# Kernel tuning notes

Hardware: AMD Instinct MI355X
Metric: run time of the kernel (lower is better)

The kernel has to match this reference:

```python
import jax, jax.numpy as jnp
import numpy as np

B, T, F, H, K = 512, 128, 256, 512, 3

def setup_inputs() -> dict:
    key = jax.random.key(0)
    ks = jax.random.split(key, 8)
    x = jax.random.normal(ks[0], (B, T, F), dtype=jnp.float32)
    theta = jnp.ones((F,), dtype=jnp.float32)                 # selector logits
    Wx = jax.random.normal(ks[1], (F, H), dtype=jnp.float32) * 0.1
    Wh = jax.random.normal(ks[2], (H, H), dtype=jnp.float32) * 0.1
    b = jnp.zeros((H,), dtype=jnp.float32)
    c = jax.random.normal(ks[3], (H, K), dtype=jnp.float32)   # fuzzy centers
    sigma = jnp.ones((H, K), dtype=jnp.float32)               # fuzzy widths
    q = jax.random.normal(ks[4], (H, K), dtype=jnp.float32)   # rule consequents
    Wc = jax.random.normal(ks[5], (H, 1), dtype=jnp.float32) * 0.05  # classifier
    bc = jnp.zeros((1,), dtype=jnp.float32)
    return dict(x=x, theta=theta, Wx=Wx, Wh=Wh, b=b, c=c, sigma=sigma, q=q, Wc=Wc, bc=bc)


def reference(x, theta, Wx, Wh, b, c, sigma, q, Wc, bc):
    weights = jax.nn.sigmoid(theta)                 # [F]
    xf = x * weights                                # [B,T,F]
    # x_t @ Wx is used twice per step (for z_t and new_info); precompute once for all t.
    xw = jnp.einsum('btf,fh->bth', xf, Wx)          # [B,T,H]
    new_info = jnp.tanh(xw)                         # [B,T,H]
    inv_den = 1.0 / (2.0 * sigma ** 2 + 1e-8)       # [H,K]

    def step(h, inp):
        xw_t, new_t = inp                           # [B,H], [B,H]
        z = xw_t + h @ Wh + b                       # [B,H]
        mu = jnp.exp(-(z[..., None] - c) ** 2 * inv_den)   # [B,H,K]
        g = jax.nn.sigmoid(jnp.sum(mu * q, axis=-1) / (jnp.sum(mu, axis=-1) + 1e-8))
        h = (1.0 - g) * h + g * new_t
        return h, None

    h0 = jnp.zeros((x.shape[0], Wh.shape[0]), dtype=x.dtype)
    h, _ = jax.lax.scan(step, h0, (jnp.swapaxes(xw, 0, 1), jnp.swapaxes(new_info, 0, 1)))
    logits = h @ Wc + bc                            # [B,1]
    return logits, weights
```

## Files before the change

kernel.cpp:

```cpp
#include <hip/hip_runtime.h>
#include <hip/hip_bf16.h>


#define B_  512
#define T_  128
#define F_  256
#define H_  512
#define LOG2E 1.4426950408889634f

#define XW_T_STRIDE 262144

typedef __attribute__((ext_vector_type(8))) short short8;
typedef __attribute__((ext_vector_type(4))) float float4v;
typedef __attribute__((ext_vector_type(4))) int int4i;

__device__ inline ushort f2bf(float f) {
  __hip_bfloat16 h = __float2bfloat16(f);
  return *reinterpret_cast<ushort*>(&h);
}
__device__ inline float bf2f(unsigned u) { return __uint_as_float(u << 16); }
__device__ inline float fexp2(float x) { return __builtin_amdgcn_exp2f(x); }
__device__ inline float frcp(float x) { return __builtin_amdgcn_rcpf(x); }

#define WS_W2I8 67108864
#define WS_WXF  67371008
#define WS_GP8  67633152
#define WS_BVEC 67649536
#define WS_WCV  67651584
#define WS_SCOL 67653632
#define WS_WTS  67657728

__global__ __launch_bounds__(256) void prep_weights(
    const float* __restrict__ Wh, const float* __restrict__ Wx,
    const float* __restrict__ theta, const float* __restrict__ b,
    const float* __restrict__ c, const float* __restrict__ sigma,
    const float* __restrict__ q, const float* __restrict__ Wc,
    int* __restrict__ W2, ushort* __restrict__ WxF,
    float* __restrict__ scol, float* __restrict__ out_w,
    float* __restrict__ gp8, float* __restrict__ bvec,
    float* __restrict__ wcv, float* __restrict__ wts) {
  __shared__ float lds[16544];
  const int t = threadIdx.x;

  if (blockIdx.x < 32) {
    const int nb = blockIdx.x;
    const int cc = t & 15, rg = t >> 4;
    float m = 0.f;
#pragma unroll
    for (int s = 0; s < 32; ++s)
      m = fmaxf(m, fabsf(Wh[(rg + s * 16) * H_ + nb * 16 + cc]));
    lds[rg * 16 + cc] = m;
    __syncthreads();
    if (t < 16) {
      float mm = lds[t];
#pragma unroll
      for (int s = 1; s < 16; ++s) mm = fmaxf(mm, lds[s * 16 + t]);
      mm = fmaxf(mm, 1e-20f);
      scol[nb * 16 + t] = mm / (127.f * 127.f);
      lds[256 + t] = 127.f / mm;
    }
    __syncthreads();
    const int lane = t & 63, dw = t >> 6;
    const int n = nb * 16 + (lane & 15);
    const float iv = lds[256 + (lane & 15)];
#pragma unroll
    for (int kt = 0; kt < 8; ++kt) {
      int pk = 0;
#pragma unroll
      for (int jj = 0; jj < 4; ++jj) {
        const int k = kt * 64 + ((lane >> 4) << 4) + dw * 4 + jj;
        int qv = (int)rintf(Wh[k * H_ + n] * iv);
        qv = min(127, max(-127, qv));
        pk |= (qv & 255) << (8 * jj);
      }
      W2[((kt * 32 + nb) * 64 + lane) * 4 + dw] = pk;
    }
  } else if (blockIdx.x < 40) {
    const int kt = blockIdx.x - 32;
#pragma unroll
    for (int it = 0; it < 16; ++it) {
      const int lin = (it * 256 + t) * 4;
      const float4 v = *(const float4*)(Wx + kt * 32 * H_ + lin);
      const int f = lin >> 9, n0 = lin & 511;
      lds[f * 517 + n0 + 0] = v.x;
      lds[f * 517 + n0 + 1] = v.y;
      lds[f * 517 + n0 + 2] = v.z;
      lds[f * 517 + n0 + 3] = v.w;
    }
    __syncthreads();
#pragma unroll
    for (int it = 0; it < 8; ++it) {
      const int o = (it * 256 + t) * 8;
      const int lane = (o >> 3) & 63, nb = o >> 9;
      const int n = nb * 16 + (lane & 15), fb = (lane >> 4) << 3;
      ushort v[8];
#pragma unroll
      for (int j = 0; j < 8; ++j) v[j] = f2bf(lds[(fb + j) * 517 + n]);
      *(short8*)(WxF + kt * 16384 + o) = *(short8*)v;
    }
  } else {
#pragma unroll
    for (int r = 0; r < 2; ++r) {
      const int i = t + r * 256;
      if (i < F_) {
        float w = 1.f / (1.f + __expf(-theta[i]));
        out_w[i] = w;
        wts[i] = w;
      }
      float a[3], cc[3], qq[3];
#pragma unroll
      for (int k = 0; k < 3; ++k) {
        float s = sigma[i * 3 + k];
        cc[k] = c[i * 3 + k];
        a[k] = -LOG2E / (2.f * s * s + 1e-8f);
        qq[k] = q[i * 3 + k];
      }
      gp8[i * 8 + 0] = cc[0];
      gp8[i * 8 + 1] = cc[1];
      gp8[i * 8 + 2] = cc[2];
      gp8[i * 8 + 3] = a[0];
      gp8[i * 8 + 4] = a[1];
      gp8[i * 8 + 5] = a[2];
      gp8[i * 8 + 6] = __uint_as_float((unsigned)f2bf(qq[0]) |
                                       ((unsigned)f2bf(qq[1]) << 16));
      gp8[i * 8 + 7] = __uint_as_float((unsigned)f2bf(qq[2]));
      bvec[i] = b[i];
      wcv[i] = Wc[i];
    }
  }
}

__global__ __launch_bounds__(256, 1) void gemm1_kernel(
    const float* __restrict__ x, const float* __restrict__ wts,
    const ushort* __restrict__ WxF, ushort* __restrict__ xw2) {
  __shared__ ushort A[64 * 264];
  const int tid = threadIdx.x;
  const int lane = tid & 63, wg = tid >> 6;
  const int col16 = lane & 15, quad = lane >> 4;
  const int tt = blockIdx.x, bb = blockIdx.y;

  {
    const float4 wv = *(const float4*)(wts + lane * 4);
#pragma unroll
    for (int it = 0; it < 16; ++it) {
      const int row = it * 4 + wg;
      float4 xv = *(const float4*)(x + ((size_t)(bb * 64 + row) * T_ + tt) * F_ + lane * 4);
      ushort4 o;
      o.x = f2bf(xv.x * wv.x);
      o.y = f2bf(xv.y * wv.y);
      o.z = f2bf(xv.z * wv.z);
      o.w = f2bf(xv.w * wv.w);
      *(ushort4*)&A[row * 264 + lane * 4] = o;
    }
  }
  __syncthreads();

  const float4v zero = {0.f, 0.f, 0.f, 0.f};
#pragma unroll
  for (int nn = 0; nn < 2; ++nn) {
    float4v acc[16];
#pragma unroll
    for (int i = 0; i < 16; ++i) acc[i] = zero;
#pragma unroll
    for (int kt = 0; kt < 8; ++kt) {
      short8 af = *(const short8*)&A[(wg * 16 + col16) * 264 + kt * 32 + quad * 8];
      short8 bfv[16];
#pragma unroll
      for (int nt = 0; nt < 16; ++nt)
        bfv[nt] = *(const short8*)(WxF + ((kt * 32 + nn * 16 + nt) * 64 + lane) * 8);
#pragma unroll
      for (int nt = 0; nt < 16; ++nt)
        acc[nt] = __builtin_amdgcn_mfma_f32_16x16x32_bf16(af, bfv[nt], acc[nt], 0, 0, 0);
    }
#pragma unroll
    for (int nt = 0; nt < 16; ++nt) {
      ushort2 lo, hi;
      lo.x = f2bf(acc[nt][0]);
      lo.y = f2bf(acc[nt][1]);
      hi.x = f2bf(acc[nt][2]);
      hi.y = f2bf(acc[nt][3]);
      const int bg0 = bb * 32 + wg * 8 + quad * 2;
      const size_t off0 =
          (((size_t)tt * 256 + bg0) * 8 + nn * 4 + (nt >> 2)) * 128 +
          ((nt & 3) * 16 + col16) * 2;
      *(ushort2*)(xw2 + off0) = lo;
      *(ushort2*)(xw2 + off0 + 1024) = hi;
    }
  }
}

__global__ __launch_bounds__(512, 2) void scan4_kernel(
    const ushort* __restrict__ xw2, const int4i* __restrict__ W2,
    const float* __restrict__ gp8, const float* __restrict__ bvec,
    const float* __restrict__ wcv, const float* __restrict__ scol,
    const float* __restrict__ bc, float* __restrict__ out) {
  __shared__ __align__(16) char hb[2][1152];
  __shared__ float red[8][2];
  const int tid = threadIdx.x;
  const int lane = tid & 63, w = tid >> 6;
  const int col16 = lane & 15, quad = lane >> 4;
  const int bg = blockIdx.x;

  for (int i = tid; i < 576; i += 512) ((int*)hb)[i] = 0;

  int4i bfr[8][4];
#pragma unroll
  for (int kt = 0; kt < 8; ++kt)
#pragma unroll
    for (int nt = 0; nt < 4; ++nt)
      bfr[kt][nt] = W2[(kt * 32 + w * 4 + nt) * 64 + lane];

  const int col = w * 64 + lane;
  const float bcol = bvec[col], scl = scol[col], wcl = wcv[col];
  float4v g0 = *(const float4v*)(gp8 + col * 8);
  float4v g1 = *(const float4v*)(gp8 + col * 8 + 4);
  const float c0v = g0[0], c1v = g0[1], c2v = g0[2];
  const float a0v = g0[3], a1v = g1[0], a2v = g1[1];
  unsigned p01 = __float_as_uint(g1[2]);
  const float q0v = bf2f(p01 & 0xffffu);
  const float q1v = bf2f(p01 >> 16);
  const float q2v = bf2f(__float_as_uint(g1[3]) & 0xffffu);
  const float b0v = -2.f * a0v * c0v, d0v = a0v * c0v * c0v;
  const float b1v = -2.f * a1v * c1v, d1v = a1v * c1v * c1v;
  const float b2v = -2.f * a2v * c2v, d2v = a2v * c2v * c2v;

  const unsigned wsel = (lane & 1) ? 0x0501u : 0x0004u;
  const int woff = col + ((lane & 1) ? 575 : 0);

  float hreg[2] = {0.f, 0.f};
  const int4i izero = {0, 0, 0, 0};
  int4i areg[8];
#pragma unroll
  for (int kt = 0; kt < 8; ++kt) areg[kt] = izero;

  const ushort* xwb = xw2 + ((size_t)bg * 8 + w) * 128 + lane * 2;
  unsigned xv = *(const unsigned*)xwb;
  unsigned xn;
  __syncthreads();

#pragma clang loop unroll(disable)
  for (int t = 0; t < T_; ++t) {
    const int tn = (t + 1) & 127;
    xn = *(const unsigned*)(xwb + (size_t)tn * XW_T_STRIDE);

    if (col16 < 2) {
      const char* abase = hb[t & 1] + col16 * 576;
#pragma unroll
      for (int kt = 0; kt < 8; ++kt)
        areg[kt] = *(const int4i*)(abase + kt * 64 + (quad << 4));
    }

    int4i acc0 = izero, acc1 = izero;
#pragma unroll
    for (int kt = 0; kt < 8; ++kt) {
      acc0 = __builtin_amdgcn_mfma_i32_16x16x64_i8(areg[kt], bfr[kt][0], acc0, 0, 0, 0);
      acc1 = __builtin_amdgcn_mfma_i32_16x16x64_i8(areg[kt], bfr[kt][1], acc1, 0, 0, 0);
    }
    int t0[2], t1[2];
#pragma unroll
    for (int rg = 0; rg < 2; ++rg) {
      t0[rg] = __shfl(acc0[rg], col16, 64);
      t1[rg] = __shfl(acc1[rg], col16, 64);
    }
    int4i acc2 = izero, acc3 = izero;
#pragma unroll
    for (int kt = 0; kt < 8; ++kt) {
      acc2 = __builtin_amdgcn_mfma_i32_16x16x64_i8(areg[kt], bfr[kt][2], acc2, 0, 0, 0);
      acc3 = __builtin_amdgcn_mfma_i32_16x16x64_i8(areg[kt], bfr[kt][3], acc3, 0, 0, 0);
    }
    int t2[2], t3[2];
#pragma unroll
    for (int rg = 0; rg < 2; ++rg) {
      t2[rg] = __shfl(acc2[rg], col16, 64);
      t3[rg] = __shfl(acc3[rg], col16, 64);
    }

    int accq[2];
#pragma unroll
    for (int rg = 0; rg < 2; ++rg) {
      int sA = (quad & 1) ? t1[rg] : t0[rg];
      int sB = (quad & 1) ? t3[rg] : t2[rg];
      accq[rg] = (quad & 2) ? sB : sA;
    }

    int qb[2];
#pragma unroll
    for (int rg = 0; rg < 2; ++rg) {
      float v = __uint_as_float(rg ? (xv & 0xffff0000u) : (xv << 16));
      float z = v + bcol + (float)accq[rg] * scl;
      float e = fexp2(v * (2.f * LOG2E));
      float nw = 1.f - 2.f * frcp(1.f + e);
      float zz = z * z;
      float m0 = fexp2(fmaf(a0v, zz, fmaf(b0v, z, d0v)));
      float m1 = fexp2(fmaf(a1v, zz, fmaf(b1v, z, d1v)));
      float m2 = fexp2(fmaf(a2v, zz, fmaf(b2v, z, d2v)));
      float num = m0 * q0v + m1 * q1v + m2 * q2v;
      float den = m0 + m1 + m2 + 1e-8f;
      float s = num * frcp(den);
      float gg = frcp(1.f + fexp2(-s * LOG2E));
      float h = hreg[rg] + gg * (nw - hreg[rg]);
      hreg[rg] = h;
      qb[rg] = (int)rintf(h * 127.f);
    }

    if (t < T_ - 1) {
      int pk = (int)__builtin_amdgcn_perm((unsigned)qb[1], (unsigned)qb[0], 0x0400u);
      unsigned p1 = (unsigned)__shfl_xor(pk, 1, 64);
      unsigned v16 = __builtin_amdgcn_perm((unsigned)pk, p1, wsel);
      *(ushort*)(hb[(t + 1) & 1] + woff) = (ushort)v16;
      __syncthreads();
    }
    xv = xn;
  }

  float part[2];
#pragma unroll
  for (int rg = 0; rg < 2; ++rg) {
    part[rg] = hreg[rg] * wcl;
#pragma unroll
    for (int m = 1; m < 64; m <<= 1) part[rg] += __shfl_xor(part[rg], m, 64);
  }
  if (lane == 0) {
    red[w][0] = part[0];
    red[w][1] = part[1];
  }
  __syncthreads();
  if (tid < 2) {
    float s = bc[0];
#pragma unroll
    for (int ww = 0; ww < 8; ++ww) s += red[ww][tid];
    out[bg * 2 + tid] = s;
  }
}

extern "C" void kernel_launch(void* const* d_in, const int* in_sizes, int n_in,
                              void* d_out, int out_size, void* d_ws, size_t ws_size,
                              hipStream_t stream) {
  const float* x     = (const float*)d_in[0];
  const float* theta = (const float*)d_in[1];
  const float* Wx    = (const float*)d_in[2];
  const float* Wh    = (const float*)d_in[3];
  const float* b     = (const float*)d_in[4];
  const float* c     = (const float*)d_in[5];
  const float* sigma = (const float*)d_in[6];
  const float* q     = (const float*)d_in[7];
  const float* Wc    = (const float*)d_in[8];
  const float* bc    = (const float*)d_in[9];
  float* out = (float*)d_out;

  ushort* xw2 = (ushort*)d_ws;
  int*    W2  = (int*)((char*)d_ws + WS_W2I8);
  ushort* WxF = (ushort*)((char*)d_ws + WS_WXF);
  float*  gp8 = (float*)((char*)d_ws + WS_GP8);
  float*  bv  = (float*)((char*)d_ws + WS_BVEC);
  float*  wcv = (float*)((char*)d_ws + WS_WCV);
  float*  scl = (float*)((char*)d_ws + WS_SCOL);
  float*  wts = (float*)((char*)d_ws + WS_WTS);

  hipLaunchKernelGGL(prep_weights, dim3(41), dim3(256), 0, stream,
                     Wh, Wx, theta, b, c, sigma, q, Wc,
                     W2, WxF, scl, out + B_, gp8, bv, wcv, wts);
  hipLaunchKernelGGL(gemm1_kernel, dim3(128, 8), dim3(256), 0, stream,
                     x, wts, WxF, xw2);
  hipLaunchKernelGGL(scan4_kernel, dim3(256), dim3(512), 0, stream,
                     xw2, (const int4i*)W2, gp8, bv, wcv, scl, bc, out);
}
```

Baseline: 266.3 us.

## Process two timesteps per gemm1 block to reuse Wx fragments, swizzle LDS

Each gemm1 block now loads x for two timesteps (t and t+64) and reuses each loaded Wx B-fragment for two MFMA chains, halving global reads of Wx per output. The LDS tile drops its padding in favour of an XOR swizzle to avoid bank conflicts. The grid is halved and launch bounds are raised to two blocks per CU. The cost is double the accumulator registers (32 float4), which may spill or limit occupancy. The scan kernel, which likely dominates total time, is untouched.

```diff
diff --git a/kernel.cpp b/kernel.cpp
--- a/kernel.cpp
+++ b/kernel.cpp
@@ -130,61 +130,76 @@
   }
 }
 
-__global__ __launch_bounds__(256, 1) void gemm1_kernel(
+__global__ __launch_bounds__(256, 2) void gemm1_kernel(
     const float* __restrict__ x, const float* __restrict__ wts,
     const ushort* __restrict__ WxF, ushort* __restrict__ xw2) {
-  __shared__ ushort A[64 * 264];
+  __shared__ ushort A2[2][64][256];
   const int tid = threadIdx.x;
   const int lane = tid & 63, wg = tid >> 6;
   const int col16 = lane & 15, quad = lane >> 4;
-  const int tt = blockIdx.x, bb = blockIdx.y;
+  const int tt2 = blockIdx.x, bb = blockIdx.y;
 
   {
     const float4 wv = *(const float4*)(wts + lane * 4);
 #pragma unroll
-    for (int it = 0; it < 16; ++it) {
-      const int row = it * 4 + wg;
-      float4 xv = *(const float4*)(x + ((size_t)(bb * 64 + row) * T_ + tt) * F_ + lane * 4);
-      ushort4 o;
-      o.x = f2bf(xv.x * wv.x);
-      o.y = f2bf(xv.y * wv.y);
-      o.z = f2bf(xv.z * wv.z);
-      o.w = f2bf(xv.w * wv.w);
-      *(ushort4*)&A[row * 264 + lane * 4] = o;
+    for (int s = 0; s < 2; ++s) {
+      const int t = tt2 + s * 64;
+#pragma unroll
+      for (int it = 0; it < 16; ++it) {
+        const int row = it * 4 + wg;
+        float4 xv = *(const float4*)(x + ((size_t)(bb * 64 + row) * T_ + t) * F_ + lane * 4);
+        ushort4 o;
+        o.x = f2bf(xv.x * wv.x);
+        o.y = f2bf(xv.y * wv.y);
+        o.z = f2bf(xv.z * wv.z);
+        o.w = f2bf(xv.w * wv.w);
+        const int ki = (lane * 4) ^ ((row & 7) << 3);
+        *(ushort4*)&A2[s][row][ki] = o;
+      }
     }
   }
   __syncthreads();
 
   const float4v zero = {0.f, 0.f, 0.f, 0.f};
+  const int arow = wg * 16 + col16;
 #pragma unroll
   for (int nn = 0; nn < 2; ++nn) {
-    float4v acc[16];
-#pragma unroll
-    for (int i = 0; i < 16; ++i) acc[i] = zero;
+    float4v acc0[16], acc1[16];
+#pragma unroll
+    for (int i = 0; i < 16; ++i) { acc0[i] = zero; acc1[i] = zero; }
 #pragma unroll
     for (int kt = 0; kt < 8; ++kt) {
-      short8 af = *(const short8*)&A[(wg * 16 + col16) * 264 + kt * 32 + quad * 8];
       short8 bfv[16];
 #pragma unroll
       for (int nt = 0; nt < 16; ++nt)
         bfv[nt] = *(const short8*)(WxF + ((kt * 32 + nn * 16 + nt) * 64 + lane) * 8);
-#pragma unroll
-      for (int nt = 0; nt < 16; ++nt)
-        acc[nt] = __builtin_amdgcn_mfma_f32_16x16x32_bf16(af, bfv[nt], acc[nt], 0, 0, 0);
-    }
-#pragma unroll
-    for (int nt = 0; nt < 16; ++nt) {
-      ushort2 lo, hi;
-      lo.x = f2bf(acc[nt][0]);
-      lo.y = f2bf(acc[nt][1]);
-      hi.x = f2bf(acc[nt][2]);
-      hi.y = f2bf(acc[nt][3]);
-      const int bg0 = bb * 32 + wg * 8 + quad * 2;
-      const size_t off0 =
-          (((size_t)tt * 256 + bg0) * 8 + nn * 4 + (nt >> 2)) * 128 +
-          ((nt & 3) * 16 + col16) * 2;
-      *(ushort2*)(xw2 + off0) = lo;
-      *(ushort2*)(xw2 + off0 + 1024) = hi;
+      const int ki = (kt * 32 + quad * 8) ^ ((arow & 7) << 3);
+      short8 af0 = *(const short8*)&A2[0][arow][ki];
+      short8 af1 = *(const short8*)&A2[1][arow][ki];
+#pragma unroll
+      for (int nt = 0; nt < 16; ++nt) {
+        acc0[nt] = __builtin_amdgcn_mfma_f32_16x16x32_bf16(af0, bfv[nt], acc0[nt], 0, 0, 0);
+        acc1[nt] = __builtin_amdgcn_mfma_f32_16x16x32_bf16(af1, bfv[nt], acc1[nt], 0, 0, 0);
+      }
+    }
+#pragma unroll
+    for (int s = 0; s < 2; ++s) {
+      const int t = tt2 + s * 64;
+#pragma unroll
+      for (int nt = 0; nt < 16; ++nt) {
+        const float4v a = s ? acc1[nt] : acc0[nt];
+        ushort2 lo, hi;
+        lo.x = f2bf(a[0]);
+        lo.y = f2bf(a[1]);
+        hi.x = f2bf(a[2]);
+        hi.y = f2bf(a[3]);
+        const int bg0 = bb * 32 + wg * 8 + quad * 2;
+        const size_t off0 =
+            (((size_t)t * 256 + bg0) * 8 + nn * 4 + (nt >> 2)) * 128 +
+            ((nt & 3) * 16 + col16) * 2;
+        *(ushort2*)(xw2 + off0) = lo;
+        *(ushort2*)(xw2 + off0 + 1024) = hi;
+      }
     }
   }
 }
@@ -360,7 +375,7 @@
   hipLaunchKernelGGL(prep_weights, dim3(41), dim3(256), 0, stream,
                      Wh, Wx, theta, b, c, sigma, q, Wc,
                      W2, WxF, scl, out + B_, gp8, bv, wcv, wts);
-  hipLaunchKernelGGL(gemm1_kernel, dim3(128, 8), dim3(256), 0, stream,
+  hipLaunchKernelGGL(gemm1_kernel, dim3(64, 8), dim3(256), 0, stream,
                      x, wts, WxF, xw2);
   hipLaunchKernelGGL(scan4_kernel, dim3(256), dim3(512), 0, stream,
                      xw2, (const int4i*)W2, gp8, bv, wcv, scl, bc, out);
```

Result: faster. 250.5 us (-5.9%).
